# Performance work log

Measured on AMD Instinct MI355X. Metric: run time of the kernel, lower is better.

## Reference

```python
import jax, jax.numpy as jnp
import numpy as np
from jax import lax

E = 8          # num_experts
K = 2          # top-k
TASKS = 8
GATE_DIM = 16
# (in, expand, out, kernel, stride) per MoE stage
STAGES = [(3, 32, 16, 7, 2), (16, 64, 32, 3, 1), (32, 128, 64, 3, 2), (64, 256, 64, 3, 1), (64, 128, 32, 3, 1)]
DN = ('NCHW', 'OIHW', 'NCHW')


def _pw(x, w):
    return lax.conv_general_dilated(x, w, (1, 1), 'VALID', dimension_numbers=DN)


def _dw(x, w, s):
    p = w.shape[-1] // 2
    return lax.conv_general_dilated(x, w, (s, s), [(p, p), (p, p)], dimension_numbers=DN, feature_group_count=x.shape[1])


def _gn(x, scale, bias):
    # GroupNorm with num_groups = C // 4, eps = 1e-5 (torch default)
    B, C, H, W = x.shape
    G = C // 4
    xr = x.reshape(B, G, -1)
    m = xr.mean(-1, keepdims=True)
    v = xr.var(-1, keepdims=True)
    xn = ((xr - m) * lax.rsqrt(v + 1e-5)).reshape(B, C, H, W)
    return xn * scale[None, :, None, None] + bias[None, :, None, None]


def _dsc(x, p, stride):
    # DSCBlock: pw-conv -> GN -> SiLU -> dw-conv -> GN -> SiLU -> pw-conv -> GN
    w1, s1, b1, w2, s2, b2, w3, s3, b3 = p
    x = jax.nn.silu(_gn(_pw(x, w1), s1, b1))
    x = jax.nn.silu(_gn(_dw(x, w2, stride), s2, b2))
    return _gn(_pw(x, w3), s3, b3)


def _moe(gate_input, x, wg, p, stride, task_bh):
    # task-conditioned top-k softmax gating (noisy_gating=False, all aux loss weights 0)
    logits = gate_input @ wg[task_bh]                      # (B, E)
    probs = jax.nn.softmax(logits, axis=-1)
    topv, topi = lax.top_k(probs, K)
    topv = topv / topv.sum(-1, keepdims=True)              # renormalize top-k gates
    Bn = gate_input.shape[0]
    dense = jnp.zeros_like(probs).at[jnp.arange(Bn)[:, None], topi].set(topv)
    eo = jax.vmap(lambda pe: _dsc(x, pe, stride))(p)       # (E, B, C, H, W)
    return jnp.einsum('be,ebchw->bchw', dense, eo)


def _forward(fl, task_bh):
    gi, xi, ppe = fl[0], fl[1], fl[2]
    x = xi
    for i, (_, _, _, _, s) in enumerate(STAGES):
        base = 3 + i * 10
        wg = fl[base]
        p = tuple(fl[base + 1: base + 10])
        x = _moe(gi, x, wg, p, s, task_bh)
    Bn = x.shape[0]
    # patchify: (B,32,20,20) -> unfold(2,4,4).unfold(3,4,4) -> permute -> (B,25,512)
    patches = x.reshape(Bn, 32, 5, 4, 5, 4).transpose(0, 1, 2, 4, 3, 5)  # (B,32,5,5,4,4)
    patches = patches.transpose(0, 2, 3, 4, 5, 1).reshape(Bn, 25, 512)
    return patches + ppe


def setup_inputs():
    key = jax.random.key(0)
    ks = iter(jax.random.split(key, 256))
    B = 64
    d = {}
    d['gate_input'] = jax.random.normal(next(ks), (B, GATE_DIM), jnp.float32)
    d['expert_input'] = jax.random.normal(next(ks), (B, 3, 80, 80), jnp.float32)
    d['patch_pos_embed'] = 0.02 * jax.random.normal(next(ks), (1, 25, 512), jnp.float32)
    for i, (cin, exp, cout, k, s) in enumerate(STAGES, 1):
        d[f's{i}_wg'] = 0.1 * jax.random.normal(next(ks), (TASKS, GATE_DIM, E), jnp.float32)
        d[f's{i}_w1'] = jax.random.normal(next(ks), (E, exp, cin, 1, 1), jnp.float32) / np.sqrt(cin)
        d[f's{i}_g1s'] = 1.0 + 0.1 * jax.random.normal(next(ks), (E, exp), jnp.float32)
        d[f's{i}_g1b'] = 0.1 * jax.random.normal(next(ks), (E, exp), jnp.float32)
        d[f's{i}_w2'] = jax.random.normal(next(ks), (E, exp, 1, k, k), jnp.float32) / k
        d[f's{i}_g2s'] = 1.0 + 0.1 * jax.random.normal(next(ks), (E, exp), jnp.float32)
        d[f's{i}_g2b'] = 0.1 * jax.random.normal(next(ks), (E, exp), jnp.float32)
        d[f's{i}_w3'] = jax.random.normal(next(ks), (E, cout, exp, 1, 1), jnp.float32) / np.sqrt(exp)
        d[f's{i}_g3s'] = 1.0 + 0.1 * jax.random.normal(next(ks), (E, cout), jnp.float32)
        d[f's{i}_g3b'] = 0.1 * jax.random.normal(next(ks), (E, cout), jnp.float32)
    d['task_bh'] = 3
    return d


def reference(gate_input, expert_input, patch_pos_embed, s1_wg, s1_w1, s1_g1s, s1_g1b, s1_w2, s1_g2s, s1_g2b, s1_w3, s1_g3s, s1_g3b, s2_wg, s2_w1, s2_g1s, s2_g1b, s2_w2, s2_g2s, s2_g2b, s2_w3, s2_g3s, s2_g3b, s3_wg, s3_w1, s3_g1s, s3_g1b, s3_w2, s3_g2s, s3_g2b, s3_w3, s3_g3s, s3_g3b, s4_wg, s4_w1, s4_g1s, s4_g1b, s4_w2, s4_g2s, s4_g2b, s4_w3, s4_g3s, s4_g3b, s5_wg, s5_w1, s5_g1s, s5_g1b, s5_w2, s5_g2s, s5_g2b, s5_w3, s5_g3s, s5_g3b, task_bh):
    fl = (gate_input, expert_input, patch_pos_embed,
          s1_wg, s1_w1, s1_g1s, s1_g1b, s1_w2, s1_g2s, s1_g2b, s1_w3, s1_g3s, s1_g3b,
          s2_wg, s2_w1, s2_g1s, s2_g1b, s2_w2, s2_g2s, s2_g2b, s2_w3, s2_g3s, s2_g3b,
          s3_wg, s3_w1, s3_g1s, s3_g1b, s3_w2, s3_g2s, s3_g2b, s3_w3, s3_g3s, s3_g3b,
          s4_wg, s4_w1, s4_g1s, s4_g1b, s4_w2, s4_g2s, s4_g2b, s4_w3, s4_g3s, s4_g3b,
          s5_wg, s5_w1, s5_g1s, s5_g1b, s5_w2, s5_g2s, s5_g2b, s5_w3, s5_g3s, s5_g3b)
    patches = _forward(fl, task_bh)
    loss = jnp.zeros((), patches.dtype)  # all MoE loss weights are 0 in VisionEncoder
    return (patches, loss)
```

## Files before the change

### kernel.cpp

```cpp
#include <hip/hip_runtime.h>
#include <cstddef>

#define TPB 256

typedef __attribute__((ext_vector_type(8))) short short8v;
typedef __attribute__((ext_vector_type(4))) float f32x4;

__device__ __forceinline__ int rfl(int v) { return __builtin_amdgcn_readfirstlane(v); }
__device__ __forceinline__ float rflf(float v) {
    return __int_as_float(__builtin_amdgcn_readfirstlane(__float_as_int(v)));
}

__device__ __forceinline__ unsigned short f2bf(float f) {
    union { float f; unsigned int u; } x{f};
    unsigned int r = x.u + 0x7fffu + ((x.u >> 16) & 1u);
    return (unsigned short)(r >> 16);
}
__device__ __forceinline__ float bf2f(unsigned short u) {
    return __uint_as_float(((unsigned int)u) << 16);
}

template <int N, int NW>
__device__ __forceinline__ void bredN(float* v, float* red) {
    __syncthreads();
    #pragma unroll
    for (int off = 32; off > 0; off >>= 1)
        #pragma unroll
        for (int i = 0; i < N; i++) v[i] += __shfl_down(v[i], off);
    const int lane = threadIdx.x & 63;
    const int wv = threadIdx.x >> 6;
    if (lane == 0)
        #pragma unroll
        for (int i = 0; i < N; i++) red[wv * N + i] = v[i];
    __syncthreads();
    if (threadIdx.x == 0) {
        #pragma unroll
        for (int i = 0; i < N; i++) {
            float s = 0.f;
            #pragma unroll
            for (int w = 0; w < NW; w++) s += red[w * N + i];
            red[i] = s;
        }
    }
    __syncthreads();
    #pragma unroll
    for (int i = 0; i < N; i++) v[i] = red[i];
}

__device__ __forceinline__ float silu_f(float v) {
    return v * __builtin_amdgcn_rcpf(1.f + __expf(-v));
}

struct GatePtrs { const float* wg[5]; };
struct WSrcs { const float* p[9]; };

__global__ __launch_bounds__(256) void wprep(WSrcs wsrc,
                                             unsigned short* __restrict__ whi) {
    const int sizes[9] = {4096, 8192, 16384, 32768, 65536, 131072, 131072, 65536, 32768};
    int idx = blockIdx.x * 256 + threadIdx.x;
    if (idx >= 487424) return;
    int rem = idx, s = 0;
    while (s < 8 && rem >= sizes[s]) { rem -= sizes[s]; s++; }
    whi[idx] = f2bf(wsrc.p[s][rem]);
}

__global__ void gate_kernel(const float* __restrict__ gi, GatePtrs gp,
                            const int* __restrict__ taskp,
                            int* __restrict__ gidx, float* __restrict__ gw) {
    const int s = blockIdx.x;
    const int b = threadIdx.x;
    const int task = taskp[0];
    const float* wg = gp.wg[s] + (size_t)task * 16 * 8;
    float l[8];
    #pragma unroll
    for (int e = 0; e < 8; e++) l[e] = 0.f;
    for (int d = 0; d < 16; d++) {
        float v = gi[b * 16 + d];
        #pragma unroll
        for (int e = 0; e < 8; e++) l[e] += v * wg[d * 8 + e];
    }
    float mx = l[0];
    #pragma unroll
    for (int e = 1; e < 8; e++) mx = fmaxf(mx, l[e]);
    float p[8]; float sum = 0.f;
    #pragma unroll
    for (int e = 0; e < 8; e++) { p[e] = expf(l[e] - mx); sum += p[e]; }
    int i0 = 0;
    #pragma unroll
    for (int e = 1; e < 8; e++) if (p[e] > p[i0]) i0 = e;
    int i1 = (i0 == 0) ? 1 : 0;
    #pragma unroll
    for (int e = 0; e < 8; e++) if (e != i0 && p[e] > p[i1]) i1 = e;
    const float denom = p[i0] + p[i1];
    const int base = (s * 64 + b) * 2;
    gidx[base] = i0; gidx[base + 1] = i1;
    gw[base] = p[i0] / denom; gw[base + 1] = p[i1] / denom;
}

template <int M, int K, int N, int MT, int NCHK, bool FOLD, bool BIN>
__global__ __launch_bounds__(256) void gemm_bf16(
    const unsigned short* __restrict__ inp,
    const unsigned short* __restrict__ whi,
    const int* __restrict__ gidx, const float* __restrict__ foldStats,
    const float* __restrict__ foldS, const float* __restrict__ foldB,
    unsigned short* __restrict__ outp, float* __restrict__ stats,
    int mfull, int moff) {
    constexpr int KITERS = (K + 31) / 32;
    constexpr int IM = (MT == 64) ? 2 : 1;
    constexpr int IN = (MT == 16) ? 1 : 2;
    const int bx = blockIdx.x;
    const int nc = bx % NCHK, mc = bx / NCHK;
    const int b = blockIdx.y, slot = blockIdx.z;
    const int bs = b * 2 + slot;
    const int e = rfl(gidx[b * 2 + slot]);
    const int n0 = nc * 64, m0 = mc * MT;
    const int tid = threadIdx.x;
    const int lane = tid & 63, wv = tid >> 6;
    const int quad = lane >> 4, l15 = lane & 15;

    __shared__ __align__(16) unsigned short wtile[MT * 40];
    __shared__ unsigned int intile[16 * 65];
    __shared__ float sred[(MT / 4) * 2];
    __shared__ float afv[K], bfv[K];

    if (tid < (MT / 4) * 2) sred[tid] = 0.f;
    if constexpr (FOLD) {
        for (int c = tid; c < K; c += 256) {
            const int g = c >> 2;
            const float s1 = foldStats[((size_t)bs * (K / 4) + g) * 2 + 0];
            const float s2 = foldStats[((size_t)bs * (K / 4) + g) * 2 + 1];
            const float mean = s1 / (4.f * N);
            const float var = s2 / (4.f * N) - mean * mean;
            const float inv = rsqrtf(var + 1e-5f);
            const float sc = foldS[e * K + c], bi = foldB[e * K + c];
            afv[c] = inv * sc;
            bfv[c] = bi - mean * inv * sc;
        }
    }

    int mbase, nbase;
    if constexpr (MT == 64) { mbase = (wv & 1) * 32; nbase = (wv >> 1) * 32; }
    else if constexpr (MT == 32) { mbase = (wv & 1) * 16; nbase = (wv >> 1) * 32; }
    else { mbase = 0; nbase = wv * 16; }

    f32x4 acc[IM][IN];
    #pragma unroll
    for (int im = 0; im < IM; im++)
        #pragma unroll
        for (int in = 0; in < IN; in++)
            #pragma unroll
            for (int r = 0; r < 4; r++) acc[im][in][r] = 0.f;

    const unsigned short* ib = inp + (size_t)(BIN ? b : bs) * K * N;
    const unsigned short* wbH = whi + ((size_t)e * mfull + moff) * K;

    for (int k0 = 0; k0 < KITERS * 32; k0 += 32) {
        __syncthreads();
        for (int i = tid; i < MT * 32; i += 256) {
            const int m = i >> 5, kk = i & 31;
            const bool ok = (k0 + kk < K);
            wtile[m * 40 + kk] = ok ? wbH[(size_t)(m0 + m) * K + k0 + kk]
                                    : (unsigned short)0;
        }
        {
            const int kp = tid >> 4, nq = tid & 15;
            const int k = k0 + kp * 2;
            const int n = n0 + nq * 4;
            unsigned short u0[4] = {0, 0, 0, 0}, u1[4] = {0, 0, 0, 0};
            const bool nv = (n < N);
            if (nv && k < K) {
                const ushort4 t = *(const ushort4*)(ib + (size_t)k * N + n);
                u0[0] = t.x; u0[1] = t.y; u0[2] = t.z; u0[3] = t.w;
            }
            if (nv && k + 1 < K) {
                const ushort4 t = *(const ushort4*)(ib + (size_t)(k + 1) * N + n);
                u1[0] = t.x; u1[1] = t.y; u1[2] = t.z; u1[3] = t.w;
            }
            #pragma unroll
            for (int t = 0; t < 4; t++) {
                float f0, f1;
                if constexpr (FOLD) {
                    f0 = (nv && k < K) ? silu_f(afv[k] * bf2f(u0[t]) + bfv[k]) : 0.f;
                    f1 = (nv && k + 1 < K) ? silu_f(afv[k + 1] * bf2f(u1[t]) + bfv[k + 1]) : 0.f;
                } else {
                    f0 = bf2f(u0[t]); f1 = bf2f(u1[t]);
                }
                intile[kp * 65 + nq * 4 + t] =
                    (unsigned int)f2bf(f0) | ((unsigned int)f2bf(f1) << 16);
            }
        }
        __syncthreads();

        short8v afr[IM];
        #pragma unroll
        for (int im = 0; im < IM; im++) {
            const int m = mbase + im * 16 + l15;
            afr[im] = *(const short8v*)&wtile[m * 40 + quad * 8];
        }
        #pragma unroll
        for (int in = 0; in < IN; in++) {
            union { unsigned int u[4]; short8v s; } bu;
            const int col = nbase + in * 16 + l15;
            #pragma unroll
            for (int i = 0; i < 4; i++) bu.u[i] = intile[(quad * 4 + i) * 65 + col];
            #pragma unroll
            for (int im = 0; im < IM; im++)
                acc[im][in] = __builtin_amdgcn_mfma_f32_16x16x32_bf16(
                    afr[im], bu.s, acc[im][in], 0, 0, 0);
        }
    }

    unsigned short* ob = outp + (size_t)bs * M * N;
    #pragma unroll
    for (int im = 0; im < IM; im++) {
        #pragma unroll
        for (int in = 0; in < IN; in++) {
            const int n = n0 + nbase + in * 16 + l15;
            float s1 = 0.f, s2 = 0.f;
            #pragma unroll
            for (int r = 0; r < 4; r++) {
                const float a = acc[im][in][r];
                s1 += a; s2 += a * a;
            }
            if (n < N) {
                #pragma unroll
                for (int r = 0; r < 4; r++) {
                    const int m = m0 + mbase + im * 16 + quad * 4 + r;
                    ob[(size_t)m * N + n] = f2bf(acc[im][in][r]);
                }
            }
            #pragma unroll
            for (int off = 8; off > 0; off >>= 1) {
                s1 += __shfl_down(s1, off, 16);
                s2 += __shfl_down(s2, off, 16);
            }
            if (l15 == 0) {
                const int gl = (mbase + im * 16) / 4 + quad;
                atomicAdd(&sred[gl * 2 + 0], s1);
                atomicAdd(&sred[gl * 2 + 1], s2);
            }
        }
    }
    __syncthreads();
    for (int i = tid; i < MT / 4; i += 256) {
        float* sp = stats + (((size_t)bs * (mfull / 4) + moff / 4 + mc * (MT / 4) + i)
                             * NCHK + nc) * 2;
        sp[0] = sred[i * 2]; sp[1] = sred[i * 2 + 1];
    }
}

template <int CLOC, int CFULL, int H, int W, int NCH, int TPBk, int NCHK1>
__global__ __launch_bounds__(TPBk) void dw_k(
    const unsigned short* __restrict__ raw1, const float* __restrict__ stats1,
    const float* __restrict__ g1s, const float* __restrict__ g1b,
    const float* __restrict__ w2, const int* __restrict__ gidx,
    unsigned short* __restrict__ act2raw, float* __restrict__ stats2, int coff) {
    constexpr int HW = H * W, HP = H + 2, WPL = W + 3;
    constexpr int NPV = HW / 4, NG = NCH / 4, NW = TPBk / 64;
    constexpr int Qc = HW / 4, QT = NCH * Qc, QI = (QT + TPBk - 1) / TPBk;
    constexpr int G1 = CFULL / 4;
    const int gch = blockIdx.x, b = blockIdx.y, slot = blockIdx.z;
    const int bs = b * 2 + slot;
    const int tid = threadIdx.x;
    const int e = rfl(gidx[b * 2 + slot]);
    const int cb0 = gch * NCH;
    const int cg0 = coff + cb0;

    __shared__ float buf1[NCH * HP * WPL];
    __shared__ float w2s[NCH * 9];
    __shared__ float afl[NCH], bfl[NCH];
    __shared__ float red[2 * NG * NW];

    for (int i = tid; i < NCH * HP * WPL; i += TPBk) buf1[i] = 0.f;
    if (tid < NCH * 9) w2s[tid] = w2[((size_t)e * CFULL + cg0) * 9 + tid];
    if (tid < NCH) {
        const int g = (cg0 + tid) >> 2;
        float s1 = 0.f, s2 = 0.f;
        for (int i = 0; i < NCHK1; i++) {
            s1 += stats1[(((size_t)bs * G1 + g) * NCHK1 + i) * 2 + 0];
            s2 += stats1[(((size_t)bs * G1 + g) * NCHK1 + i) * 2 + 1];
        }
        const float mean = s1 / (4.f * HW);
        const float var = s2 / (4.f * HW) - mean * mean;
        const float inv = rsqrtf(var + 1e-5f);
        const float sc = g1s[e * CFULL + cg0 + tid], bi = g1b[e * CFULL + cg0 + tid];
        afl[tid] = inv * sc; bfl[tid] = bi - mean * inv * sc;
    }
    __syncthreads();

    const unsigned short* rb = raw1 + (size_t)bs * CLOC * HW + (size_t)cb0 * HW;
    for (int i = tid; i < NCH * NPV; i += TPBk) {
        const int c = i / NPV, pv = i - c * NPV;
        const int p4 = pv * 4, ph = p4 / W, pwb = p4 - ph * W;
        const ushort4 u = *(const ushort4*)(rb + (size_t)c * HW + p4);
        const float a = afl[c], bb = bfl[c];
        float* bp = &buf1[(c * HP + ph + 1) * WPL + pwb + 1];
        bp[0] = silu_f(a * bf2f(u.x) + bb);
        bp[1] = silu_f(a * bf2f(u.y) + bb);
        bp[2] = silu_f(a * bf2f(u.z) + bb);
        bp[3] = silu_f(a * bf2f(u.w) + bb);
    }
    __syncthreads();

    float st2[2 * NG];
    #pragma unroll
    for (int i = 0; i < 2 * NG; i++) st2[i] = 0.f;
    unsigned short* ao = act2raw + (size_t)bs * CFULL * HW + (size_t)cg0 * HW;
    #pragma unroll
    for (int qi = 0; qi < QI; qi++) {
        const int q = tid + qi * TPBk;
        if (QI * TPBk == QT || q < QT) {
            const int c = q / Qc, qq = q - c * Qc;
            const int oh = qq % H, owb = (qq / H) * 4;
            float o[4] = {0.f, 0.f, 0.f, 0.f};
            #pragma unroll
            for (int kh = 0; kh < 3; kh++) {
                const int base = (c * HP + oh + kh) * WPL + owb;
                float r[6];
                #pragma unroll
                for (int i = 0; i < 6; i++) r[i] = buf1[base + i];
                const float wa = w2s[c * 9 + kh * 3 + 0];
                const float wb = w2s[c * 9 + kh * 3 + 1];
                const float wcc = w2s[c * 9 + kh * 3 + 2];
                #pragma unroll
                for (int t = 0; t < 4; t++)
                    o[t] += wa * r[t] + wb * r[t + 1] + wcc * r[t + 2];
            }
            ushort4 ov = {f2bf(o[0]), f2bf(o[1]), f2bf(o[2]), f2bf(o[3])};
            *(ushort4*)(ao + c * HW + oh * W + owb) = ov;
            #pragma unroll
            for (int t = 0; t < 4; t++) {
                if constexpr (NG == 1) { st2[0] += o[t]; st2[1] += o[t] * o[t]; }
                else {
                    const bool gs = (c >= 4);
                    float a0 = gs ? 0.f : o[t], a1 = gs ? o[t] : 0.f;
                    st2[0] += a0; st2[1] += a0 * a0;
                    st2[2] += a1; st2[3] += a1 * a1;
                }
            }
        }
    }
    bredN<2 * NG, NW>(st2, red);
    if (tid == 0) {
        #pragma unroll
        for (int g = 0; g < NG; g++) {
            stats2[((size_t)bs * G1 + cg0 / 4 + g) * 2 + 0] = st2[g * 2];
            stats2[((size_t)bs * G1 + cg0 / 4 + g) * 2 + 1] = st2[g * 2 + 1];
        }
    }
}

__global__ __launch_bounds__(256) void s1_stats(
    const float* __restrict__ xin, const float* __restrict__ w1,
    const int* __restrict__ gidx, float* __restrict__ stats1) {
    const int g = blockIdx.x, b = blockIdx.y, slot = blockIdx.z;
    const int tid = threadIdx.x;
    const int e = rfl(gidx[b * 2 + slot]);
    __shared__ float red[8];
    const float* xb = xin + (size_t)b * 3 * 6400;
    const float* w1e = w1 + ((size_t)e * 32 + g * 4) * 3;
    float wr[4][3];
    #pragma unroll
    for (int c = 0; c < 4; c++)
        #pragma unroll
        for (int k = 0; k < 3; k++) wr[c][k] = rflf(w1e[c * 3 + k]);
    float s[2] = {0.f, 0.f};
    #pragma unroll
    for (int j = 0; j < 7; j++) {
        const int i = j * 256 + tid;
        if (i < 1600) {
            const int p4 = i * 4;
            const float4 v0 = *(const float4*)(xb + p4);
            const float4 v1 = *(const float4*)(xb + 6400 + p4);
            const float4 v2 = *(const float4*)(xb + 12800 + p4);
            const float a0[4] = {v0.x, v0.y, v0.z, v0.w};
            const float a1[4] = {v1.x, v1.y, v1.z, v1.w};
            const float a2[4] = {v2.x, v2.y, v2.z, v2.w};
            #pragma unroll
            for (int t = 0; t < 4; t++)
                #pragma unroll
                for (int c = 0; c < 4; c++) {
                    float a = fmaf(wr[c][0], a0[t], fmaf(wr[c][1], a1[t], wr[c][2] * a2[t]));
                    s[0] += a; s[1] += a * a;
                }
        }
    }
    bredN<2, 4>(s, red);
    if (tid == 0) {
        float* sp = stats1 + ((size_t)(b * 2 + slot) * 8 + g) * 2;
        sp[0] = s[0]; sp[1] = s[1];
    }
}

__global__ __launch_bounds__(256) void s1_band(
    const float* __restrict__ xin, const float* __restrict__ w1,
    const float* __restrict__ g1s, const float* __restrict__ g1b,
    const float* __restrict__ w2, const int* __restrict__ gidx,
    const float* __restrict__ stats1,
    float* __restrict__ rawdw, float* __restrict__ stats2) {
    constexpr int NR = 25, RW = 90, EVO = 44;
    const int gb = blockIdx.x;
    const int g = gb >> 2, band = gb & 3;
    const int b = blockIdx.y, slot = blockIdx.z;
    const int tid = threadIdx.x;
    const int e = rfl(gidx[b * 2 + slot]);

    __shared__ float sbuf[4 * NR * RW];
    __shared__ float w2s[196];
    __shared__ float red[8];

    for (int i = tid; i < 4 * NR * RW; i += 256) sbuf[i] = 0.f;
    if (tid < 196) w2s[tid] = w2[((size_t)e * 32 + g * 4) * 49 + tid];

    const float* sp = stats1 + ((size_t)(b * 2 + slot) * 8 + g) * 2;
    const float s1v = rflf(sp[0]), s2v = rflf(sp[1]);
    const float mean = s1v / 25600.f;
    const float var = s2v / 25600.f - mean * mean;
    const float inv = rsqrtf(var + 1e-5f);

    const float* xb = xin + (size_t)b * 3 * 6400;
    const float* w1e = w1 + ((size_t)e * 32 + g * 4) * 3;
    float wr[4][3], sc1r[4], bi1r[4];
    #pragma unroll
    for (int c = 0; c < 4; c++) {
        #pragma unroll
        for (int k = 0; k < 3; k++) wr[c][k] = rflf(w1e[c * 3 + k]);
        sc1r[c] = rflf(g1s[e * 32 + g * 4 + c]);
        bi1r[c] = rflf(g1b[e * 32 + g * 4 + c]);
    }
    const int oh0 = band * 10;
    const int rlo = 2 * oh0 - 3;
    __syncthreads();

    for (int ii = tid; ii < 500; ii += 256) {
        const int p4 = ii * 4;
        const int l = p4 / 80, pw = p4 - l * 80;
        const int r = rlo + l;
        if (r >= 0 && r < 80) {
            const float4 v0 = *(const float4*)(xb + r * 80 + pw);
            const float4 v1 = *(const float4*)(xb + 6400 + r * 80 + pw);
            const float4 v2 = *(const float4*)(xb + 12800 + r * 80 + pw);
            const float a0[4] = {v0.x, v0.y, v0.z, v0.w};
            const float a1[4] = {v1.x, v1.y, v1.z, v1.w};
            const float a2[4] = {v2.x, v2.y, v2.z, v2.w};
            #pragma unroll
            for (int c = 0; c < 4; c++) {
                #pragma unroll
                for (int t = 0; t < 4; t++) {
                    float a = fmaf(wr[c][0], a0[t], fmaf(wr[c][1], a1[t], wr[c][2] * a2[t]));
                    float v = silu_f((a - mean) * inv * sc1r[c] + bi1r[c]);
                    const int cc = pw + t + 3;
                    const int sl = (cc & 1) ? EVO + (cc >> 1) : (cc >> 1);
                    sbuf[(c * NR + l) * RW + sl] = v;
                }
            }
        }
    }
    __syncthreads();

    float st2[2] = {0.f, 0.f};
    float* rw = rawdw + (size_t)(b * 2 + slot) * 32 * 1600 + (size_t)g * 4 * 1600;
    #pragma unroll
    for (int qi = 0; qi < 2; qi++) {
        const int q = tid + qi * 256;
        if (q < 400) {
            const int c = q / 100;
            const int rem = q - c * 100;
            const int ohl = rem % 10, owb = (rem / 10) * 4;
            float o[4] = {0.f, 0.f, 0.f, 0.f};
            #pragma unroll
            for (int kh = 0; kh < 7; kh++) {
                const int base = (c * NR + 2 * ohl + kh) * RW;
                const float2 e01 = *(const float2*)&sbuf[base + owb];
                const float2 e23 = *(const float2*)&sbuf[base + owb + 2];
                const float2 e45 = *(const float2*)&sbuf[base + owb + 4];
                const float e6 = sbuf[base + owb + 6];
                const float2 q01 = *(const float2*)&sbuf[base + EVO + owb];
                const float2 q23 = *(const float2*)&sbuf[base + EVO + owb + 2];
                const float2 q45 = *(const float2*)&sbuf[base + EVO + owb + 4];
                const float evr[7] = {e01.x, e01.y, e23.x, e23.y, e45.x, e45.y, e6};
                const float odr[6] = {q01.x, q01.y, q23.x, q23.y, q45.x, q45.y};
                const float w0 = w2s[c * 49 + kh * 7 + 0];
                const float w1v = w2s[c * 49 + kh * 7 + 1];
                const float w2v = w2s[c * 49 + kh * 7 + 2];
                const float w3 = w2s[c * 49 + kh * 7 + 3];
                const float w4 = w2s[c * 49 + kh * 7 + 4];
                const float w5 = w2s[c * 49 + kh * 7 + 5];
                const float w6 = w2s[c * 49 + kh * 7 + 6];
                #pragma unroll
                for (int t = 0; t < 4; t++)
                    o[t] += w0 * evr[t] + w1v * odr[t] + w2v * evr[t + 1]
                          + w3 * odr[t + 1] + w4 * evr[t + 2] + w5 * odr[t + 2]
                          + w6 * evr[t + 3];
            }
            const int oh = oh0 + ohl;
            float4 ov = {o[0], o[1], o[2], o[3]};
            *(float4*)(rw + c * 1600 + oh * 40 + owb) = ov;
            #pragma unroll
            for (int t = 0; t < 4; t++) { st2[0] += o[t]; st2[1] += o[t] * o[t]; }
        }
    }
    bredN<2, 4>(st2, red);
    if (tid == 0) {
        float* s2p = stats2 + (((size_t)(b * 2 + slot) * 8 + g) * 4 + band) * 2;
        s2p[0] = st2[0]; s2p[1] = st2[1];
    }
}

__global__ __launch_bounds__(256) void s1_norm(
    const float* __restrict__ rawdw, const float* __restrict__ stats2,
    const float* __restrict__ g2s, const float* __restrict__ g2b,
    const int* __restrict__ gidx, unsigned short* __restrict__ act2) {
    const int g = blockIdx.x, b = blockIdx.y, slot = blockIdx.z;
    const int tid = threadIdx.x;
    const int e = rfl(gidx[b * 2 + slot]);
    const float* sp = stats2 + ((size_t)(b * 2 + slot) * 8 + g) * 8;
    const float s1 = rflf(sp[0]) + rflf(sp[2]) + rflf(sp[4]) + rflf(sp[6]);
    const float s2 = rflf(sp[1]) + rflf(sp[3]) + rflf(sp[5]) + rflf(sp[7]);
    const float mean2 = s1 / 6400.f;
    const float var2 = s2 / 6400.f - mean2 * mean2;
    const float inv2 = rsqrtf(var2 + 1e-5f);
    const float* rb = rawdw + (size_t)(b * 2 + slot) * 32 * 1600 + (size_t)g * 4 * 1600;
    unsigned short* ao = act2 + ((size_t)(b * 2 + slot) * 32 + g * 4) * 1600;
    #pragma unroll
    for (int c = 0; c < 4; c++) {
        const float sc = rflf(g2s[e * 32 + g * 4 + c]);
        const float bi = rflf(g2b[e * 32 + g * 4 + c]);
        #pragma unroll
        for (int qi = 0; qi < 2; qi++) {
            const int i = tid + qi * 256;
            if (i < 400) {
                const float4 v = *(const float4*)(rb + c * 1600 + i * 4);
                ushort4 ov;
                ov.x = f2bf(silu_f((v.x - mean2) * inv2 * sc + bi));
                ov.y = f2bf(silu_f((v.y - mean2) * inv2 * sc + bi));
                ov.z = f2bf(silu_f((v.z - mean2) * inv2 * sc + bi));
                ov.w = f2bf(silu_f((v.w - mean2) * inv2 * sc + bi));
                *(ushort4*)(ao + c * 1600 + i * 4) = ov;
            }
        }
    }
}

template <int CIN, int CEXP, int KS, int STRIDE, int H, int W, int HO, int WO,
          int NCH, int TPBk>
__global__ __launch_bounds__(TPBk) void dsc_ab_v2(
    const unsigned short* __restrict__ xin, const float* __restrict__ w1,
    const float* __restrict__ g1s, const float* __restrict__ g1b,
    const float* __restrict__ w2,
    const float* __restrict__ g2s, const float* __restrict__ g2b,
    const int* __restrict__ gidx, unsigned short* __restrict__ act2) {
    constexpr int HW = H * W, HWO = HO * WO;
    constexpr int HP = H + 2, WPL = W + 3, EVW = (W + 2) / 2;
    constexpr int NPV = HW / 4;
    constexpr int JN = (NPV + TPBk - 1) / TPBk;
    constexpr int NW = TPBk / 64;
    constexpr int NG = NCH / 4;
    constexpr int Qc = HWO / 4;
    constexpr int QT = NCH * Qc;
    constexpr int QI = (QT + TPBk - 1) / TPBk;
    constexpr int KK = KS * KS;
    const int gch = blockIdx.x, b = blockIdx.y, slot = blockIdx.z;
    const int tid = threadIdx.x;
    const int e = rfl(gidx[b * 2 + slot]);
    const int cb0 = gch * NCH;

    __shared__ float buf1[NCH * HP * WPL];
    __shared__ float w2s[NCH * KK];
    __shared__ float sc2s[NCH], bi2s[NCH];
    __shared__ float red[2 * NG * NW];

    for (int i = tid; i < NCH * HP * WPL; i += TPBk) buf1[i] = 0.f;
    for (int i = tid; i < NCH * KK; i += TPBk) {
        int c = i / KK, k = i - c * KK;
        w2s[i] = w2[((size_t)e * CEXP + cb0 + c) * KK + k];
    }
    if (tid < NCH) {
        sc2s[tid] = g2s[e * CEXP + cb0 + tid];
        bi2s[tid] = g2b[e * CEXP + cb0 + tid];
    }

    const unsigned short* xb = xin + (size_t)b * CIN * HW;
    const float* w1e = w1 + ((size_t)e * CEXP + cb0) * CIN;

    float acc[NCH][JN][4];
    #pragma unroll
    for (int c = 0; c < NCH; c++)
        #pragma unroll
        for (int j = 0; j < JN; j++)
            #pragma unroll
            for (int t = 0; t < 4; t++) acc[c][j][t] = 0.f;

    for (int cb = 0; cb < CIN; cb += 4) {
        float wr[NCH][4];
        #pragma unroll
        for (int c = 0; c < NCH; c++)
            #pragma unroll
            for (int k = 0; k < 4; k++) wr[c][k] = rflf(w1e[c * CIN + cb + k]);
        #pragma unroll
        for (int j = 0; j < JN; j++) {
            const int pv = tid + j * TPBk;
            if (JN * TPBk == NPV || pv < NPV) {
                #pragma unroll
                for (int k = 0; k < 4; k++) {
                    const ushort4 v4 = *(const ushort4*)(xb + (cb + k) * HW + pv * 4);
                    const float va[4] = {bf2f(v4.x), bf2f(v4.y), bf2f(v4.z), bf2f(v4.w)};
                    #pragma unroll
                    for (int c = 0; c < NCH; c++)
                        #pragma unroll
                        for (int t = 0; t < 4; t++)
                            acc[c][j][t] = fmaf(wr[c][k], va[t], acc[c][j][t]);
                }
            }
        }
    }
    float st[2 * NG];
    #pragma unroll
    for (int i = 0; i < 2 * NG; i++) st[i] = 0.f;
    #pragma unroll
    for (int c = 0; c < NCH; c++) {
        const int gs = (c >> 2) * 2;
        #pragma unroll
        for (int j = 0; j < JN; j++)
            #pragma unroll
            for (int t = 0; t < 4; t++) {
                float a = acc[c][j][t];
                st[gs] += a; st[gs + 1] += a * a;
            }
    }
    bredN<2 * NG, NW>(st, red);
    float mg[NG], ig[NG];
    #pragma unroll
    for (int g = 0; g < NG; g++) {
        mg[g] = st[g * 2] / (4.f * HW);
        float var = st[g * 2 + 1] / (4.f * HW) - mg[g] * mg[g];
        ig[g] = rsqrtf(var + 1e-5f);
    }
    float sc1r[NCH], bi1r[NCH];
    #pragma unroll
    for (int c = 0; c < NCH; c++) {
        sc1r[c] = rflf(g1s[e * CEXP + cb0 + c]);
        bi1r[c] = rflf(g1b[e * CEXP + cb0 + c]);
    }
    #pragma unroll
    for (int j = 0; j < JN; j++) {
        const int pv = tid + j * TPBk;
        if (JN * TPBk == NPV || pv < NPV) {
            const int p4 = pv * 4;
            const int ph = p4 / W, pwb = p4 - ph * W;
            #pragma unroll
            for (int c = 0; c < NCH; c++) {
                const int g = (NG == 1) ? 0 : (c >> 2);
                #pragma unroll
                for (int t = 0; t < 4; t++) {
                    float v = silu_f((acc[c][j][t] - mg[g]) * ig[g] * sc1r[c] + bi1r[c]);
                    const int j2 = pwb + t + 1;
                    const int col = (STRIDE == 1) ? j2
                                    : ((j2 & 1) ? EVW + (j2 >> 1) : (j2 >> 1));
                    buf1[(c * HP + ph + 1) * WPL + col] = v;
                }
            }
        }
    }
    __syncthreads();

    float dacc[QI][4];
    float st2[2 * NG];
    #pragma unroll
    for (int i = 0; i < 2 * NG; i++) st2[i] = 0.f;
    #pragma unroll
    for (int qi = 0; qi < QI; qi++) {
        #pragma unroll
        for (int t = 0; t < 4; t++) dacc[qi][t] = 0.f;
        const int q = tid + qi * TPBk;
        if (QI * TPBk == QT || q < QT) {
            const int c = q / Qc, qq = q - c * Qc;
            const int oh = qq % HO, owb = (qq / HO) * 4;
            float o[4] = {0.f, 0.f, 0.f, 0.f};
            if (STRIDE == 1) {
                #pragma unroll
                for (int kh = 0; kh < KS; kh++) {
                    const int base = (c * HP + oh + kh) * WPL + owb;
                    float r[6];
                    #pragma unroll
                    for (int i = 0; i < 6; i++) r[i] = buf1[base + i];
                    const float wa = w2s[c * KK + kh * KS + 0];
                    const float wb = w2s[c * KK + kh * KS + 1];
                    const float wcc = w2s[c * KK + kh * KS + 2];
                    #pragma unroll
                    for (int t = 0; t < 4; t++)
                        o[t] += wa * r[t] + wb * r[t + 1] + wcc * r[t + 2];
                }
            } else {
                #pragma unroll
                for (int kh = 0; kh < KS; kh++) {
                    const int base = (c * HP + 2 * oh + kh) * WPL;
                    float ev[5], od[4];
                    #pragma unroll
                    for (int i = 0; i < 5; i++) ev[i] = buf1[base + owb + i];
                    #pragma unroll
                    for (int i = 0; i < 4; i++) od[i] = buf1[base + EVW + owb + i];
                    const float wa = w2s[c * KK + kh * KS + 0];
                    const float wb = w2s[c * KK + kh * KS + 1];
                    const float wcc = w2s[c * KK + kh * KS + 2];
                    #pragma unroll
                    for (int t = 0; t < 4; t++)
                        o[t] += wa * ev[t] + wb * od[t] + wcc * ev[t + 1];
                }
            }
            #pragma unroll
            for (int t = 0; t < 4; t++) {
                float a = o[t];
                dacc[qi][t] = a;
                if constexpr (NG == 1) {
                    st2[0] += a; st2[1] += a * a;
                } else {
                    const bool gsel = (c >= 4);
                    float a0 = gsel ? 0.f : a, a1 = gsel ? a : 0.f;
                    st2[0] += a0; st2[1] += a0 * a0;
                    st2[2] += a1; st2[3] += a1 * a1;
                }
            }
        }
    }
    bredN<2 * NG, NW>(st2, red);
    float m2[NG], i2[NG];
    #pragma unroll
    for (int g = 0; g < NG; g++) {
        m2[g] = st2[g * 2] / (4.f * HWO);
        float var = st2[g * 2 + 1] / (4.f * HWO) - m2[g] * m2[g];
        i2[g] = rsqrtf(var + 1e-5f);
    }
    unsigned short* ao = act2 + ((size_t)(b * 2 + slot) * CEXP + cb0) * HWO;
    #pragma unroll
    for (int qi = 0; qi < QI; qi++) {
        const int q = tid + qi * TPBk;
        if (QI * TPBk == QT || q < QT) {
            const int c = q / Qc, qq = q - c * Qc;
            const int oh = qq % HO, owb = (qq / HO) * 4;
            const int g = (NG == 1) ? 0 : ((c >= 4) ? 1 : 0);
            const float sc = sc2s[c], bi = bi2s[c];
            ushort4 ov;
            ov.x = f2bf(silu_f((dacc[qi][0] - m2[g]) * i2[g] * sc + bi));
            ov.y = f2bf(silu_f((dacc[qi][1] - m2[g]) * i2[g] * sc + bi));
            ov.z = f2bf(silu_f((dacc[qi][2] - m2[g]) * i2[g] * sc + bi));
            ov.w = f2bf(silu_f((dacc[qi][3] - m2[g]) * i2[g] * sc + bi));
            *(ushort4*)(ao + c * HWO + oh * WO + owb) = ov;
        }
    }
}

template <int COUT, int HWO, int PXC, bool PATCH>
__global__ __launch_bounds__(256) void pw3_k3m(
    const unsigned short* __restrict__ raw3, const float* __restrict__ statsw,
    const float* __restrict__ g3s, const float* __restrict__ g3b,
    const int* __restrict__ gidx, const float* __restrict__ gw,
    const float* __restrict__ ppe, float* __restrict__ outf,
    unsigned short* __restrict__ outb) {
    constexpr int G = COUT / 4;
    constexpr int Q = HWO / 4;
    const int gg = blockIdx.x, b = blockIdx.y;
    const int tid = threadIdx.x;

    float A[2][4], Bv[2][4];
    #pragma unroll
    for (int slot = 0; slot < 2; slot++) {
        const int e = rfl(gidx[b * 2 + slot]);
        const float wgt = rflf(gw[b * 2 + slot]);
        const float* sp = statsw + ((size_t)(b * 2 + slot) * G + gg) * PXC * 2;
        float s1 = 0.f, s2 = 0.f;
        for (int i = 0; i < PXC; i++) { s1 += rflf(sp[i * 2]); s2 += rflf(sp[i * 2 + 1]); }
        const float mean = s1 / (4.f * HWO);
        const float var = s2 / (4.f * HWO) - mean * mean;
        const float inv = rsqrtf(var + 1e-5f);
        #pragma unroll
        for (int i = 0; i < 4; i++) {
            const int c = gg * 4 + i;
            const float sc = rflf(g3s[e * COUT + c]);
            const float bi = rflf(g3b[e * COUT + c]);
            A[slot][i] = wgt * inv * sc;
            Bv[slot][i] = wgt * (bi - mean * inv * sc);
        }
    }

    #pragma unroll
    for (int i = 0; i < 4; i++) {
        const int c = gg * 4 + i;
        const unsigned short* r0 = raw3 + ((size_t)(b * 2 + 0) * COUT + c) * HWO;
        const unsigned short* r1 = raw3 + ((size_t)(b * 2 + 1) * COUT + c) * HWO;
        for (int q = tid; q < Q; q += 256) {
            const int p4 = q * 4;
            const ushort4 u0 = *(const ushort4*)(r0 + p4);
            const ushort4 u1 = *(const ushort4*)(r1 + p4);
            const float v0[4] = {bf2f(u0.x), bf2f(u0.y), bf2f(u0.z), bf2f(u0.w)};
            const float v1[4] = {bf2f(u1.x), bf2f(u1.y), bf2f(u1.z), bf2f(u1.w)};
            float o[4];
            #pragma unroll
            for (int t = 0; t < 4; t++)
                o[t] = fmaf(A[0][i], v0[t], Bv[0][i]) + fmaf(A[1][i], v1[t], Bv[1][i]);
            if constexpr (!PATCH) {
                ushort4 ov = {f2bf(o[0]), f2bf(o[1]), f2bf(o[2]), f2bf(o[3])};
                *(ushort4*)(outb + ((size_t)b * COUT + c) * HWO + p4) = ov;
            } else {
                const int ph = p4 / 20, pw0 = p4 - ph * 20;
                const int p = (ph >> 2) * 5 + (pw0 >> 2);
                const int dbase = ((ph & 3) * 4) * 32 + c;
                float* op = outf + ((size_t)b * 25 + p) * 512;
                const float* pp = ppe + p * 512;
                #pragma unroll
                for (int jj = 0; jj < 4; jj++)
                    op[dbase + jj * 32] = o[jj] + pp[dbase + jj * 32];
            }
        }
    }
    if (PATCH && gg == 0 && b == 0 && tid == 0) outf[64 * 25 * 512] = 0.f;
}

extern "C" void kernel_launch(void* const* d_in, const int* in_sizes, int n_in,
                              void* d_out, int out_size, void* d_ws, size_t ws_size,
                              hipStream_t stream) {
    const float* gate_input = (const float*)d_in[0];
    const float* expert_input = (const float*)d_in[1];
    const float* ppe = (const float*)d_in[2];
    const int* taskp = (const int*)d_in[53];
    auto in = [&](int s, int k) { return (const float*)d_in[3 + s * 10 + k]; };

    char* ws = (char*)d_ws;
    int* gidx = (int*)ws;
    float* gw = (float*)(ws + 4096);
    size_t off = 8192;
    unsigned short* x0 = (unsigned short*)(ws + off); off += (size_t)8 << 20;
    unsigned short* x1 = (unsigned short*)(ws + off); off += (size_t)8 << 20;
    unsigned short* act2 = (unsigned short*)(ws + off); off += (size_t)27 << 20;
    char* bufA = ws + off; off += (size_t)27 << 20;
    float* stats1 = (float*)(ws + off); off += (size_t)2 << 20;
    float* stats2 = (float*)(ws + off); off += 262144;
    float* stats3 = (float*)(ws + off); off += (size_t)1 << 20;
    float* st1a = (float*)(ws + off); off += 65536;
    float* st1b = (float*)(ws + off); off += 65536;
    unsigned short* whi = (unsigned short*)(ws + off); off += 487424 * 2;
    float* outp = (float*)d_out;
    unsigned short* bufA16 = (unsigned short*)bufA;

    WSrcs wsrc;
    wsrc.p[0] = in(0, 7); wsrc.p[1] = in(1, 1); wsrc.p[2] = in(1, 7);
    wsrc.p[3] = in(2, 1); wsrc.p[4] = in(2, 7); wsrc.p[5] = in(3, 1);
    wsrc.p[6] = in(3, 7); wsrc.p[7] = in(4, 1); wsrc.p[8] = in(4, 7);

    GatePtrs gp;
    for (int s = 0; s < 5; s++) gp.wg[s] = in(s, 0);
    gate_kernel<<<5, 64, 0, stream>>>(gate_input, gp, taskp, gidx, gw);
    wprep<<<(487424 + 255) / 256, 256, 0, stream>>>(wsrc, whi);

    s1_stats<<<dim3(8, 64, 2), 256, 0, stream>>>(expert_input, in(0, 1),
                                                 gidx + 0 * 128, st1a);
    s1_band<<<dim3(32, 64, 2), 256, 0, stream>>>(
        expert_input, in(0, 1), in(0, 2), in(0, 3), in(0, 4),
        gidx + 0 * 128, st1a, (float*)bufA, st1b);
    s1_norm<<<dim3(8, 64, 2), 256, 0, stream>>>(
        (float*)bufA, st1b, in(0, 5), in(0, 6), gidx + 0 * 128, act2);
    gemm_bf16<16, 32, 1600, 16, 25, false, false><<<dim3(25, 64, 2), 256, 0, stream>>>(
        act2, whi + 0, gidx + 0 * 128, nullptr, nullptr, nullptr,
        bufA16, stats3, 16, 0);
    pw3_k3m<16, 1600, 25, false><<<dim3(4, 64), 256, 0, stream>>>(
        bufA16, stats3, in(0, 8), in(0, 9), gidx + 0 * 128,
        gw + 0 * 128, ppe, nullptr, x0);

    gemm_bf16<64, 16, 1600, 64, 25, false, true><<<dim3(25, 64, 2), 256, 0, stream>>>(
        x0, whi + 4096, gidx + 1 * 128, nullptr, nullptr, nullptr,
        bufA16, stats1, 64, 0);
    dw_k<64, 64, 40, 40, 4, 256, 25><<<dim3(16, 64, 2), 256, 0, stream>>>(
        bufA16, stats1, in(1, 2), in(1, 3), in(1, 4),
        gidx + 1 * 128, act2, stats2, 0);
    gemm_bf16<32, 64, 1600, 32, 25, true, false><<<dim3(25, 64, 2), 256, 0, stream>>>(
        act2, whi + 12288, gidx + 1 * 128, stats2, in(1, 5), in(1, 6),
        bufA16, stats3, 32, 0);
    pw3_k3m<32, 1600, 25, false><<<dim3(8, 64), 256, 0, stream>>>(
        bufA16, stats3, in(1, 8), in(1, 9), gidx + 1 * 128,
        gw + 1 * 128, ppe, nullptr, x1);

    dsc_ab_v2<32, 128, 3, 2, 40, 40, 20, 20, 4, 256><<<dim3(32, 64, 2), 256, 0, stream>>>(
        x1, in(2, 1), in(2, 2), in(2, 3), in(2, 4), in(2, 5), in(2, 6),
        gidx + 2 * 128, act2);
    gemm_bf16<64, 128, 400, 64, 7, false, false><<<dim3(7, 64, 2), 256, 0, stream>>>(
        act2, whi + 61440, gidx + 2 * 128, nullptr, nullptr, nullptr,
        bufA16, stats3, 64, 0);
    pw3_k3m<64, 400, 7, false><<<dim3(16, 64), 256, 0, stream>>>(
        bufA16, stats3, in(2, 8), in(2, 9), gidx + 2 * 128,
        gw + 2 * 128, ppe, nullptr, x0);

    gemm_bf16<256, 64, 400, 64, 7, false, true><<<dim3(28, 64, 2), 256, 0, stream>>>(
        x0, whi + 126976, gidx + 3 * 128, nullptr, nullptr, nullptr,
        bufA16, stats1, 256, 0);
    dw_k<256, 256, 20, 20, 8, 128, 7><<<dim3(32, 64, 2), 128, 0, stream>>>(
        bufA16, stats1, in(3, 2), in(3, 3), in(3, 4),
        gidx + 3 * 128, act2, stats2, 0);
    gemm_bf16<64, 256, 400, 64, 7, true, false><<<dim3(7, 64, 2), 256, 0, stream>>>(
        act2, whi + 258048, gidx + 3 * 128, stats2, in(3, 5), in(3, 6),
        bufA16, stats3, 64, 0);
    pw3_k3m<64, 400, 7, false><<<dim3(16, 64), 256, 0, stream>>>(
        bufA16, stats3, in(3, 8), in(3, 9), gidx + 3 * 128,
        gw + 3 * 128, ppe, nullptr, x1);

    gemm_bf16<128, 64, 400, 64, 7, false, true><<<dim3(14, 64, 2), 256, 0, stream>>>(
        x1, whi + 389120, gidx + 4 * 128, nullptr, nullptr, nullptr,
        bufA16, stats1, 128, 0);
    dw_k<128, 128, 20, 20, 8, 128, 7><<<dim3(16, 64, 2), 128, 0, stream>>>(
        bufA16, stats1, in(4, 2), in(4, 3), in(4, 4),
        gidx + 4 * 128, act2, stats2, 0);
    gemm_bf16<32, 128, 400, 32, 7, true, false><<<dim3(7, 64, 2), 256, 0, stream>>>(
        act2, whi + 454656, gidx + 4 * 128, stats2, in(4, 5), in(4, 6),
        bufA16, stats3, 32, 0);
    pw3_k3m<32, 400, 7, true><<<dim3(8, 64), 256, 0, stream>>>(
        bufA16, stats3, in(4, 8), in(4, 9), gidx + 4 * 128,
        gw + 4 * 128, ppe, outp, nullptr);
}
```

Baseline: 521.7 us.

## Fuse stage-1 GN2+SiLU into GEMM fold and store dw output as bf16

```diff
diff --git a/kernel.cpp b/kernel.cpp
--- a/kernel.cpp
+++ b/kernel.cpp
@@ -104,7 +104,7 @@
     const int* __restrict__ gidx, const float* __restrict__ foldStats,
     const float* __restrict__ foldS, const float* __restrict__ foldB,
     unsigned short* __restrict__ outp, float* __restrict__ stats,
-    int mfull, int moff) {
+    int mfull, int moff, int nchk1) {
     constexpr int KITERS = (K + 31) / 32;
     constexpr int IM = (MT == 64) ? 2 : 1;
     constexpr int IN = (MT == 16) ? 1 : 2;
@@ -127,8 +127,11 @@
     if constexpr (FOLD) {
         for (int c = tid; c < K; c += 256) {
             const int g = c >> 2;
-            const float s1 = foldStats[((size_t)bs * (K / 4) + g) * 2 + 0];
-            const float s2 = foldStats[((size_t)bs * (K / 4) + g) * 2 + 1];
+            float s1 = 0.f, s2 = 0.f;
+            for (int i = 0; i < nchk1; i++) {
+                s1 += foldStats[(((size_t)bs * (K / 4) + g) * nchk1 + i) * 2 + 0];
+                s2 += foldStats[(((size_t)bs * (K / 4) + g) * nchk1 + i) * 2 + 1];
+            }
             const float mean = s1 / (4.f * N);
             const float var = s2 / (4.f * N) - mean * mean;
             const float inv = rsqrtf(var + 1e-5f);
@@ -397,8 +400,8 @@
     const float* __restrict__ g1s, const float* __restrict__ g1b,
     const float* __restrict__ w2, const int* __restrict__ gidx,
     const float* __restrict__ stats1,
-    float* __restrict__ rawdw, float* __restrict__ stats2) {
-    constexpr int NR = 25, RW = 90, EVO = 44;
+    unsigned short* __restrict__ rawdw, float* __restrict__ stats2) {
+    constexpr int NR = 25, RW = 91, EVO = 44;
     const int gb = blockIdx.x;
     const int g = gb >> 2, band = gb & 3;
     const int b = blockIdx.y, slot = blockIdx.z;
@@ -437,6 +440,7 @@
         const int l = p4 / 80, pw = p4 - l * 80;
         const int r = rlo + l;
         if (r >= 0 && r < 80) {
+            const int lrow = (l >> 1) + (l & 1) * 13;
             const float4 v0 = *(const float4*)(xb + r * 80 + pw);
             const float4 v1 = *(const float4*)(xb + 6400 + r * 80 + pw);
             const float4 v2 = *(const float4*)(xb + 12800 + r * 80 + pw);
@@ -451,7 +455,7 @@
                     float v = silu_f((a - mean) * inv * sc1r[c] + bi1r[c]);
                     const int cc = pw + t + 3;
                     const int sl = (cc & 1) ? EVO + (cc >> 1) : (cc >> 1);
-                    sbuf[(c * NR + l) * RW + sl] = v;
+                    sbuf[(c * NR + lrow) * RW + sl] = v;
                 }
             }
         }
@@ -459,7 +463,8 @@
     __syncthreads();
 
     float st2[2] = {0.f, 0.f};
-    float* rw = rawdw + (size_t)(b * 2 + slot) * 32 * 1600 + (size_t)g * 4 * 1600;
+    unsigned short* rw = rawdw + (size_t)(b * 2 + slot) * 32 * 1600
+                         + (size_t)g * 4 * 1600;
     #pragma unroll
     for (int qi = 0; qi < 2; qi++) {
         const int q = tid + qi * 256;
@@ -470,7 +475,8 @@
             float o[4] = {0.f, 0.f, 0.f, 0.f};
             #pragma unroll
             for (int kh = 0; kh < 7; kh++) {
-                const int base = (c * NR + 2 * ohl + kh) * RW;
+                const int lrow = ohl + (kh >> 1) + (kh & 1) * 13;
+                const int base = (c * NR + lrow) * RW;
                 const float2 e01 = *(const float2*)&sbuf[base + owb];
                 const float2 e23 = *(const float2*)&sbuf[base + owb + 2];
                 const float2 e45 = *(const float2*)&sbuf[base + owb + 4];
@@ -494,8 +500,8 @@
                           + w6 * evr[t + 3];
             }
             const int oh = oh0 + ohl;
-            float4 ov = {o[0], o[1], o[2], o[3]};
-            *(float4*)(rw + c * 1600 + oh * 40 + owb) = ov;
+            ushort4 ov = {f2bf(o[0]), f2bf(o[1]), f2bf(o[2]), f2bf(o[3])};
+            *(ushort4*)(rw + c * 1600 + oh * 40 + owb) = ov;
             #pragma unroll
             for (int t = 0; t < 4; t++) { st2[0] += o[t]; st2[1] += o[t] * o[t]; }
         }
@@ -504,41 +510,6 @@
     if (tid == 0) {
         float* s2p = stats2 + (((size_t)(b * 2 + slot) * 8 + g) * 4 + band) * 2;
         s2p[0] = st2[0]; s2p[1] = st2[1];
-    }
-}
-
-__global__ __launch_bounds__(256) void s1_norm(
-    const float* __restrict__ rawdw, const float* __restrict__ stats2,
-    const float* __restrict__ g2s, const float* __restrict__ g2b,
-    const int* __restrict__ gidx, unsigned short* __restrict__ act2) {
-    const int g = blockIdx.x, b = blockIdx.y, slot = blockIdx.z;
-    const int tid = threadIdx.x;
-    const int e = rfl(gidx[b * 2 + slot]);
-    const float* sp = stats2 + ((size_t)(b * 2 + slot) * 8 + g) * 8;
-    const float s1 = rflf(sp[0]) + rflf(sp[2]) + rflf(sp[4]) + rflf(sp[6]);
-    const float s2 = rflf(sp[1]) + rflf(sp[3]) + rflf(sp[5]) + rflf(sp[7]);
-    const float mean2 = s1 / 6400.f;
-    const float var2 = s2 / 6400.f - mean2 * mean2;
-    const float inv2 = rsqrtf(var2 + 1e-5f);
-    const float* rb = rawdw + (size_t)(b * 2 + slot) * 32 * 1600 + (size_t)g * 4 * 1600;
-    unsigned short* ao = act2 + ((size_t)(b * 2 + slot) * 32 + g * 4) * 1600;
-    #pragma unroll
-    for (int c = 0; c < 4; c++) {
-        const float sc = rflf(g2s[e * 32 + g * 4 + c]);
-        const float bi = rflf(g2b[e * 32 + g * 4 + c]);
-        #pragma unroll
-        for (int qi = 0; qi < 2; qi++) {
-            const int i = tid + qi * 256;
-            if (i < 400) {
-                const float4 v = *(const float4*)(rb + c * 1600 + i * 4);
-                ushort4 ov;
-                ov.x = f2bf(silu_f((v.x - mean2) * inv2 * sc + bi));
-                ov.y = f2bf(silu_f((v.y - mean2) * inv2 * sc + bi));
-                ov.z = f2bf(silu_f((v.z - mean2) * inv2 * sc + bi));
-                ov.w = f2bf(silu_f((v.w - mean2) * inv2 * sc + bi));
-                *(ushort4*)(ao + c * 1600 + i * 4) = ov;
-            }
-        }
     }
 }
 
@@ -856,25 +827,23 @@
                                                  gidx + 0 * 128, st1a);
     s1_band<<<dim3(32, 64, 2), 256, 0, stream>>>(
         expert_input, in(0, 1), in(0, 2), in(0, 3), in(0, 4),
-        gidx + 0 * 128, st1a, (float*)bufA, st1b);
-    s1_norm<<<dim3(8, 64, 2), 256, 0, stream>>>(
-        (float*)bufA, st1b, in(0, 5), in(0, 6), gidx + 0 * 128, act2);
-    gemm_bf16<16, 32, 1600, 16, 25, false, false><<<dim3(25, 64, 2), 256, 0, stream>>>(
-        act2, whi + 0, gidx + 0 * 128, nullptr, nullptr, nullptr,
-        bufA16, stats3, 16, 0);
+        gidx + 0 * 128, st1a, bufA16, st1b);
+    gemm_bf16<16, 32, 1600, 16, 25, true, false><<<dim3(25, 64, 2), 256, 0, stream>>>(
+        bufA16, whi + 0, gidx + 0 * 128, st1b, in(0, 5), in(0, 6),
+        act2, stats3, 16, 0, 4);
     pw3_k3m<16, 1600, 25, false><<<dim3(4, 64), 256, 0, stream>>>(
-        bufA16, stats3, in(0, 8), in(0, 9), gidx + 0 * 128,
+        act2, stats3, in(0, 8), in(0, 9), gidx + 0 * 128,
         gw + 0 * 128, ppe, nullptr, x0);
 
     gemm_bf16<64, 16, 1600, 64, 25, false, true><<<dim3(25, 64, 2), 256, 0, stream>>>(
         x0, whi + 4096, gidx + 1 * 128, nullptr, nullptr, nullptr,
-        bufA16, stats1, 64, 0);
+        bufA16, stats1, 64, 0, 1);
     dw_k<64, 64, 40, 40, 4, 256, 25><<<dim3(16, 64, 2), 256, 0, stream>>>(
         bufA16, stats1, in(1, 2), in(1, 3), in(1, 4),
         gidx + 1 * 128, act2, stats2, 0);
     gemm_bf16<32, 64, 1600, 32, 25, true, false><<<dim3(25, 64, 2), 256, 0, stream>>>(
         act2, whi + 12288, gidx + 1 * 128, stats2, in(1, 5), in(1, 6),
-        bufA16, stats3, 32, 0);
+        bufA16, stats3, 32, 0, 1);
     pw3_k3m<32, 1600, 25, false><<<dim3(8, 64), 256, 0, stream>>>(
         bufA16, stats3, in(1, 8), in(1, 9), gidx + 1 * 128,
         gw + 1 * 128, ppe, nullptr, x1);
@@ -884,33 +853,33 @@
         gidx + 2 * 128, act2);
     gemm_bf16<64, 128, 400, 64, 7, false, false><<<dim3(7, 64, 2), 256, 0, stream>>>(
         act2, whi + 61440, gidx + 2 * 128, nullptr, nullptr, nullptr,
-        bufA16, stats3, 64, 0);
+        bufA16, stats3, 64, 0, 1);
     pw3_k3m<64, 400, 7, false><<<dim3(16, 64), 256, 0, stream>>>(
         bufA16, stats3, in(2, 8), in(2, 9), gidx + 2 * 128,
         gw + 2 * 128, ppe, nullptr, x0);
 
     gemm_bf16<256, 64, 400, 64, 7, false, true><<<dim3(28, 64, 2), 256, 0, stream>>>(
         x0, whi + 126976, gidx + 3 * 128, nullptr, nullptr, nullptr,
-        bufA16, stats1, 256, 0);
+        bufA16, stats1, 256, 0, 1);
     dw_k<256, 256, 20, 20, 8, 128, 7><<<dim3(32, 64, 2), 128, 0, stream>>>(
         bufA16, stats1, in(3, 2), in(3, 3), in(3, 4),
         gidx + 3 * 128, act2, stats2, 0);
     gemm_bf16<64, 256, 400, 64, 7, true, false><<<dim3(7, 64, 2), 256, 0, stream>>>(
         act2, whi + 258048, gidx + 3 * 128, stats2, in(3, 5), in(3, 6),
-        bufA16, stats3, 64, 0);
+        bufA16, stats3, 64, 0, 1);
     pw3_k3m<64, 400, 7, false><<<dim3(16, 64), 256, 0, stream>>>(
         bufA16, stats3, in(3, 8), in(3, 9), gidx + 3 * 128,
         gw + 3 * 128, ppe, nullptr, x1);
 
     gemm_bf16<128, 64, 400, 64, 7, false, true><<<dim3(14, 64, 2), 256, 0, stream>>>(
         x1, whi + 389120, gidx + 4 * 128, nullptr, nullptr, nullptr,
-        bufA16, stats1, 128, 0);
+        bufA16, stats1, 128, 0, 1);
     dw_k<128, 128, 20, 20, 8, 128, 7><<<dim3(16, 64, 2), 128, 0, stream>>>(
         bufA16, stats1, in(4, 2), in(4, 3), in(4, 4),
         gidx + 4 * 128, act2, stats2, 0);
     gemm_bf16<32, 128, 400, 32, 7, true, false><<<dim3(7, 64, 2), 256, 0, stream>>>(
         act2, whi + 454656, gidx + 4 * 128, stats2, in(4, 5), in(4, 6),
-        bufA16, stats3, 32, 0);
+        bufA16, stats3, 32, 0, 1);
     pw3_k3m<32, 400, 7, true><<<dim3(8, 64), 256, 0, stream>>>(
         bufA16, stats3, in(4, 8), in(4, 9), gidx + 4 * 128,
         gw + 4 * 128, ppe, outp, nullptr);
```

Result: faster. 495.2 us (-5.1%).
